# Kernel optimization log

Hardware: AMD Instinct MI355X
Metric: run time of the kernel (lower is better)

Reference implementation:

```python
import jax, jax.numpy as jnp
import numpy as np

IMG_H, IMG_W = 1024, 1024
STRIDES = (8, 16, 32, 64, 128)
NUM_CLASSES = 80
CONF_THR = 0.05
IOU_THR = 0.5
MAX_PER_CLASS = 100
MAX_DET = 100
K_CAND = 256  # candidates kept per class before greedy NMS (pre-sort cap)


def build_grids():
    gy, gx, gs = [], [], []
    for s in STRIDES:
        H, W = IMG_H // s, IMG_W // s
        h = jnp.arange(H, dtype=jnp.float32)
        w = jnp.arange(W, dtype=jnp.float32)
        gy_, gx_ = jnp.meshgrid(h, w)  # 'xy' indexing -> shape [W, H], matches tf.meshgrid
        gy.append(gy_.reshape(-1))
        gx.append(gx_.reshape(-1))
        gs.append(jnp.full((W * H,), float(s), dtype=jnp.float32))
    return jnp.concatenate(gy), jnp.concatenate(gx), jnp.concatenate(gs)


def pairwise_iou(b):
    # b: [K,4] as (y1, x1, y2, x2)
    y1, x1, y2, x2 = b[:, 0], b[:, 1], b[:, 2], b[:, 3]
    area = (y2 - y1) * (x2 - x1)
    ih = jnp.maximum(jnp.minimum(y2[:, None], y2[None, :]) - jnp.maximum(y1[:, None], y1[None, :]), 0.0)
    iw = jnp.maximum(jnp.minimum(x2[:, None], x2[None, :]) - jnp.maximum(x1[:, None], x1[None, :]), 0.0)
    inter = ih * iw
    union = area[:, None] + area[None, :] - inter
    return inter / jnp.maximum(union, 1e-8)


def nms_one_class(boxes, scores):
    # boxes [N,4], scores [N] -> (sel_boxes [MAX_PER_CLASS,4], sel_scores [MAX_PER_CLASS])
    top_s, idx = jax.lax.top_k(scores, K_CAND)
    cand = boxes[idx]                       # [K,4]
    valid = top_s > CONF_THR
    iou = jax.lax.stop_gradient(pairwise_iou(cand))  # suppression mask is non-differentiable
    rng = jnp.arange(K_CAND)

    def body(i, keep):
        sup = (iou[i] > IOU_THR) & (rng > i) & keep[i]
        return keep & ~sup

    keep = jax.lax.fori_loop(0, K_CAND, body, valid)
    kept = jnp.where(keep, top_s, 0.0)
    sel_s, sel_i = jax.lax.top_k(kept, MAX_PER_CLASS)
    return cand[sel_i], sel_s


def combined_nms(boxes, scores):
    # per image: boxes [N,4] shared across classes, scores [N,C]
    cls_boxes, cls_scores = jax.vmap(nms_one_class, in_axes=(None, 1))(boxes, scores)
    C = scores.shape[1]
    cls_labels = jnp.broadcast_to(jnp.arange(C, dtype=jnp.float32)[:, None], cls_scores.shape)
    flat_s = cls_scores.reshape(-1)
    flat_b = cls_boxes.reshape(-1, 4)
    flat_l = cls_labels.reshape(-1)
    fin_s, fin_i = jax.lax.top_k(flat_s, MAX_DET)
    fin_b = flat_b[fin_i] * (fin_s > 0.0)[:, None].astype(flat_b.dtype)  # zero pad boxes like TF
    fin_l = flat_l[fin_i]
    return fin_b, fin_l, fin_s


def decode(pred_regs, pred_ctrs, pred_clfs):
    gy, gx, gs = build_grids()
    gy, gx, gs = gy[:, None], gx[:, None], gs[:, None]     # [N,1]
    score = pred_clfs * pred_ctrs                           # [B,N,C]
    x1 = gx - pred_regs[..., 0:1]
    x2 = gx + pred_regs[..., 1:2]
    y1 = gy - pred_regs[..., 2:3]
    y2 = gy + pred_regs[..., 3:4]
    bbox = jnp.concatenate([y1, x1, y2, x2], axis=-1) * gs  # [B,N,4] in image coords
    return jax.vmap(combined_nms)(bbox, score)


def setup_inputs() -> dict:
    key = jax.random.key(0)
    k1, k2, k3 = jax.random.split(key, 3)
    N = sum((IMG_H // s) * (IMG_W // s) for s in STRIDES)  # 21824
    B = 16
    return {
        "pred_regs": jax.random.uniform(k1, (B, N, 4), jnp.float32),
        "pred_ctrs": jax.random.uniform(k2, (B, N, 1), jnp.float32),
        "pred_clfs": jax.random.uniform(k3, (B, N, NUM_CLASSES), jnp.float32),
    }


def reference(pred_regs, pred_ctrs, pred_clfs):
    # returns (final_bboxes [B,100,4], final_labels [B,100] float, final_scores [B,100])
    return decode(pred_regs, pred_ctrs, pred_clfs)
```

## Files before the change

kernel.cpp:

```cpp
#include <hip/hip_runtime.h>
#include <stdint.h>

#pragma clang fp contract(off)

namespace {
constexpr int kN = 21824;
constexpr int kB = 16;
constexpr int kC = 80;
constexpr int kK = 256;
constexpr int kMaxPC = 100;
constexpr int kMaxDet = 100;
constexpr int kBins1 = 2048;
constexpr int kCap = 1536;
constexpr int kSortN = 512;
constexpr int kRows = kB * kC;
constexpr int kTiles = kN / 64;
constexpr int kTPB = 6;
constexpr int kGScan = (kTiles + kTPB - 1) / kTPB;
constexpr int kLCap = 48;
constexpr float kThr = 0.72f;
}

__device__ __forceinline__ uint64_t make_key(float s, int n) {
  return ((uint64_t)__float_as_uint(s) << 16) | (uint32_t)(0xFFFF - n);
}

__device__ uint32_t block_scan_incl(uint32_t val) {
  __shared__ uint32_t wsum[4];
  int lane = threadIdx.x & 63;
  int wave = threadIdx.x >> 6;
  for (int d = 1; d < 64; d <<= 1) {
    uint32_t t = __shfl_up(val, (unsigned)d, 64);
    if (lane >= d) val += t;
  }
  if (lane == 63) wsum[wave] = val;
  __syncthreads();
  uint32_t off = 0;
  for (int w = 0; w < wave; ++w) off += wsum[w];
  __syncthreads();
  return val + off;
}

struct RegSrc {
  uint64_t k[6];
  int cnt;
  template <class F> __device__ void each(F f) const {
    #pragma unroll
    for (int j = 0; j < 6; ++j)
      if (j < cnt) f(k[j]);
  }
  template <class F> __device__ void each2(F f) const {
    #pragma unroll
    for (int j = 0; j < 6; ++j) f(k[j], j < cnt);
  }
};
struct ColSrc {
  const float* cl;
  const float* ct;
  template <class F> __device__ void each(F f) const {
    for (int n = threadIdx.x; n < kN; n += 256)
      f(make_key(cl[(size_t)n * kC] * ct[n], n));
  }
  template <class F> __device__ void each2(F f) const {
    constexpr int kNr = (kN + 255) & ~255;
    for (int n = threadIdx.x; n < kNr; n += 256) {
      bool v = n < kN;
      float s = v ? cl[(size_t)n * kC] * ct[n] : 0.0f;
      f(make_key(s, n), v);
    }
  }
};
struct ArrSrc {
  const float* s;
  int count;
  template <class F> __device__ void each(F f) const {
    for (int i = threadIdx.x; i < count; i += 256) f(make_key(s[i], i));
  }
  template <class F> __device__ void each2(F f) const {
    int cr = (count + 255) & ~255;
    for (int i = threadIdx.x; i < cr; i += 256) {
      bool v = i < count;
      float sv = v ? s[i] : 0.0f;
      f(make_key(sv, i), v);
    }
  }
};

template <class Src, bool FAST>
__device__ int refine_gather(const Src& src, int K, int cap,
                             uint32_t* hist, uint64_t* cbuf) {
  __shared__ int sel_bin;
  __shared__ uint32_t sel_hd, sel_above, qcnt;
  int tid = threadIdx.x;

  for (int i = tid; i < kBins1; i += 256) hist[i] = 0;
  __syncthreads();
  src.each([&](uint64_t k) {
    uint32_t bin = FAST ? (uint32_t)((k >> 28) & 0x7FF) : (uint32_t)(k >> 37);
    atomicAdd(&hist[bin], 1u);
  });
  __syncthreads();
  uint32_t krem = (uint32_t)K;
  {
    uint32_t bl[8], v = 0;
    int base = kBins1 - 1 - 8 * tid;
    for (int j = 0; j < 8; ++j) { bl[j] = hist[base - j]; v += bl[j]; }
    uint32_t S = block_scan_incl(v);
    if (S >= krem && (S - v) < krem) {
      uint32_t cum = S - v;
      for (int j = 0; j < 8; ++j) {
        cum += bl[j];
        if (cum >= krem) { sel_bin = base - j; sel_hd = bl[j]; sel_above = cum - bl[j]; break; }
      }
    }
    __syncthreads();
  }
  uint64_t prefix = FAST ? (uint64_t)(0x3F000u | (uint32_t)sel_bin)
                         : (uint64_t)sel_bin;
  int shift = FAST ? 28 : 37;
  krem = (uint32_t)K - sel_above;
  uint32_t Sge = ((uint32_t)K - krem) + sel_hd;
  __syncthreads();

  while (Sge > (uint32_t)cap) {
    int w = (shift > 8) ? 8 : shift;
    int ns = shift - w, bins = 1 << w, hs = shift;
    for (int i = tid; i < bins; i += 256) hist[i] = 0;
    __syncthreads();
    uint64_t pfx = prefix;
    src.each([&](uint64_t k) {
      if ((k >> hs) == pfx)
        atomicAdd(&hist[(uint32_t)(k >> ns) & (bins - 1)], 1u);
    });
    __syncthreads();
    uint32_t v = (tid < bins) ? hist[bins - 1 - tid] : 0;
    uint32_t S = block_scan_incl(v);
    if (v && S >= krem && (S - v) < krem) {
      sel_bin = bins - 1 - tid; sel_hd = v; sel_above = S - v;
    }
    __syncthreads();
    prefix = (prefix << w) | (uint32_t)sel_bin;
    krem -= sel_above;
    Sge = ((uint32_t)K - krem) + sel_hd;
    shift = ns;
    __syncthreads();
  }

  uint64_t L = prefix << shift;
  if (tid == 0) qcnt = 0;
  __syncthreads();
  {
    int lane = tid & 63;
    uint64_t lmask = (1ull << lane) - 1ull;
    src.each2([&](uint64_t k, bool valid) {
      bool q = valid && (k >= L);
      unsigned long long m = __ballot(q);
      uint32_t base = 0;
      if (lane == 0 && m) base = atomicAdd(&qcnt, (uint32_t)__popcll(m));
      base = __shfl(base, 0, 64);
      if (q) {
        uint32_t p = base + (uint32_t)__popcll(m & lmask);
        if (p < (uint32_t)cap) cbuf[p] = k;
      }
    });
  }
  __syncthreads();
  int Scnt = (int)qcnt;
  return Scnt > cap ? cap : Scnt;
}

__device__ __forceinline__ void bitonic512_desc(uint64_t* sortb) {
  int tid = threadIdx.x;
  uint64_t e0 = sortb[2 * tid], e1 = sortb[2 * tid + 1];
  #pragma unroll
  for (int k2 = 2; k2 <= kSortN; k2 <<= 1) {
    #pragma unroll
    for (int j = k2 >> 1; j >= 2; j >>= 1) {
      bool up = ((tid & (k2 >> 1)) == 0);
      uint64_t p0, p1;
      bool low;
      if (j >= 128) {
        __syncthreads();
        sortb[2 * tid] = e0; sortb[2 * tid + 1] = e1;
        __syncthreads();
        int pi = (2 * tid) ^ j;
        p0 = sortb[pi]; p1 = sortb[pi + 1];
        low = ((tid & (j >> 1)) == 0);
      } else {
        int d = j >> 1;
        p0 = (uint64_t)__shfl_xor((unsigned long long)e0, d, 64);
        p1 = (uint64_t)__shfl_xor((unsigned long long)e1, d, 64);
        low = ((tid & d) == 0);
      }
      bool keepMax = (up == low);
      e0 = (keepMax == (e0 > p0)) ? e0 : p0;
      e1 = (keepMax == (e1 > p1)) ? e1 : p1;
    }
    {
      bool up = ((tid & (k2 >> 1)) == 0);
      bool sw = up ? (e0 < e1) : (e0 > e1);
      uint64_t t0 = sw ? e1 : e0, t1 = sw ? e0 : e1;
      e0 = t0; e1 = t1;
    }
  }
  __syncthreads();
  sortb[2 * tid] = e0; sortb[2 * tid + 1] = e1;
  __syncthreads();
}

__global__ __launch_bounds__(256) void score_scan_kernel(
    const float* __restrict__ clfs, const float* __restrict__ ctrs,
    uint32_t* __restrict__ gcnt, uint64_t* __restrict__ glist) {
  int b = blockIdx.y;
  int t0 = blockIdx.x * kTPB;
  int t1 = t0 + kTPB; if (t1 > kTiles) t1 = kTiles;
  int nbase = t0 * 64;
  int nanch = (t1 - t0) * 64;

  __shared__ uint64_t lbuf[kC][kLCap + 1];
  __shared__ uint32_t lcnt[kC];
  __shared__ uint32_t gbase[kC];
  __shared__ float ct[kTPB * 64];
  int tid = threadIdx.x;
  for (int i = tid; i < kC; i += 256) lcnt[i] = 0;
  for (int i = tid; i < nanch; i += 256) ct[i] = ctrs[(size_t)b * kN + nbase + i];
  __syncthreads();

  const float4* src = (const float4*)(clfs + ((size_t)b * kN + nbase) * kC);
  int n4 = nanch * (kC / 4);
  float4 v = (tid < n4) ? src[tid] : float4{0, 0, 0, 0};
  for (int e = tid; e < n4; e += 256) {
    int en = e + 256;
    float4 vn = (en < n4) ? src[en] : float4{0, 0, 0, 0};
    int a = e / 20;
    int c0 = (e % 20) * 4;
    float cv = ct[a];
    int n = nbase + a;
    float sv[4] = {v.x * cv, v.y * cv, v.z * cv, v.w * cv};
    #pragma unroll
    for (int j = 0; j < 4; ++j) {
      if (sv[j] > kThr) {
        int c = c0 + j;
        uint32_t p = atomicAdd(&lcnt[c], 1u);
        if (p < kLCap) lbuf[c][p] = make_key(sv[j], n);
      }
    }
    v = vn;
  }
  __syncthreads();

  if (tid < kC) {
    uint32_t m = lcnt[tid];
    int row = b * kC + tid;
    if (m > kLCap) {
      atomicAdd(&gcnt[row], (uint32_t)(kCap + 1));
      gbase[tid] = 0xFFFFFFFFu;
    } else {
      gbase[tid] = m ? atomicAdd(&gcnt[row], m) : 0u;
    }
  }
  __syncthreads();

  int lane = tid & 63, wave = tid >> 6;
  for (int c = wave * 20; c < wave * 20 + 20; ++c) {
    uint32_t m = lcnt[c];
    uint32_t base = gbase[c];
    if (base == 0xFFFFFFFFu || m == 0) continue;
    if (m > kLCap) m = kLCap;
    int row = b * kC + c;
    for (uint32_t i = lane; i < m; i += 64) {
      uint32_t p = base + i;
      if (p < kCap) glist[(size_t)row * kCap + p] = lbuf[c][i];
    }
  }
}

__global__ __launch_bounds__(256) void nms_class_kernel(
    const uint32_t* __restrict__ gcnt, const uint64_t* __restrict__ glist,
    const float* __restrict__ clfs, const float* __restrict__ ctrs,
    const float* __restrict__ regs,
    float* __restrict__ cls_boxes, float* __restrict__ cls_scores) {
  int row = blockIdx.x;
  int b = row / kC, c = row % kC;
  int tid = threadIdx.x;
  int lane = tid & 63, wave = tid >> 6;

  __shared__ union alignas(16) {
    uint32_t hist[kBins1];
    uint64_t sortb[kSortN];
    uint32_t supm[kK][8];
  } hu;
  __shared__ float4 boxf4[kK];
  __shared__ float barea[kK];
  __shared__ uint64_t kinit[4];
  __shared__ uint64_t kfin[4];

  uint32_t cnt = gcnt[row];
  int Scnt;
  if (cnt >= (uint32_t)kK && cnt <= (uint32_t)kCap) {
    RegSrc rs; rs.cnt = 0;
    const uint64_t* gl = glist + (size_t)row * kCap;
    #pragma unroll
    for (int j = 0; j < 6; ++j) {
      int i = tid + j * 256;
      if (i < (int)cnt) { rs.k[j] = gl[i]; rs.cnt = j + 1; }
    }
    Scnt = refine_gather<RegSrc, true>(rs, kK, kSortN, hu.hist, hu.sortb);
  } else {
    ColSrc cs{clfs + (size_t)b * kN * kC + c, ctrs + (size_t)b * kN};
    Scnt = refine_gather<ColSrc, false>(cs, kK, kSortN, hu.hist, hu.sortb);
  }

  for (int i = Scnt + tid; i < kSortN; i += 256) hu.sortb[i] = 0;
  __syncthreads();
  bitonic512_desc(hu.sortb);
  uint64_t myk = hu.sortb[tid];
  __syncthreads();

  int n = 0xFFFF - (int)(myk & 0xFFFF);
  float sc_v = __uint_as_float((uint32_t)(myk >> 16));
  int off, hl;
  float sf;
  if (n < 16384)      { off = 0;     hl = 7; sf = 8.f;   }
  else if (n < 20480) { off = 16384; hl = 6; sf = 16.f;  }
  else if (n < 21504) { off = 20480; hl = 5; sf = 32.f;  }
  else if (n < 21760) { off = 21504; hl = 4; sf = 64.f;  }
  else                { off = 21760; hl = 3; sf = 128.f; }
  int kk = n - off;
  float gx = (float)(kk >> hl);
  float gy = (float)(kk & ((1 << hl) - 1));
  const float4 r = ((const float4*)regs)[(size_t)b * kN + n];
  float4 mybox;
  mybox.x = (gy - r.z) * sf;
  mybox.y = (gx - r.x) * sf;
  mybox.z = (gy + r.w) * sf;
  mybox.w = (gx + r.y) * sf;
  float my_a = (mybox.z - mybox.x) * (mybox.w - mybox.y);
  boxf4[tid] = mybox;
  barea[tid] = my_a;
  unsigned long long vm = __ballot(sc_v > 0.05f);
  if (lane == 0) kinit[wave] = vm;
  {
    uint64_t* sp = (uint64_t*)&hu.supm[0][0];
    #pragma unroll
    for (int q = 0; q < 4; ++q) sp[tid + q * 256] = 0;
  }
  __syncthreads();

  {
    int tw = tid >> 5;
    uint32_t meq = 0xFFFFFFFEu << (tid & 31);
    for (int w = wave << 1; w < 8; ++w) {
      const float4* bp = boxf4 + (w << 5);
      const float* ap = barea + (w << 5);
      uint32_t cur = 0;
      #pragma unroll
      for (int s = 0; s < 32; ++s) {
        const float4 Bx = bp[s];
        float aB = ap[s];
        float yy1 = fmaxf(mybox.x, Bx.x);
        float yy2 = fminf(mybox.z, Bx.z);
        float xx1 = fmaxf(mybox.y, Bx.y);
        float xx2 = fminf(mybox.w, Bx.w);
        float ih = fmaxf(yy2 - yy1, 0.0f);
        float iw = fmaxf(xx2 - xx1, 0.0f);
        float inter = ih * iw;
        float un = (aB + my_a) - inter;
        float unc = fmaxf(un, 1e-8f);
        cur |= (inter + inter > unc) ? (1u << s) : 0u;
      }
      uint32_t mask = (w > tw) ? 0xFFFFFFFFu : ((w == tw) ? meq : 0u);
      if (mask) hu.supm[tid][w] = cur & mask;
    }
  }
  __syncthreads();

  if (wave == 0) {
    uint64_t kw0 = kinit[0], kw1 = kinit[1], kw2 = kinit[2], kw3 = kinit[3];
    #define NMS_SECTION(W, KW)                                              \
      _Pragma("unroll")                                                     \
      for (int ch = 0; ch < 16; ++ch) {                                     \
        const ulonglong2* s0 = (const ulonglong2*)hu.supm[(W << 6) + ch * 4 + 0]; \
        const ulonglong2* s1 = (const ulonglong2*)hu.supm[(W << 6) + ch * 4 + 1]; \
        const ulonglong2* s2 = (const ulonglong2*)hu.supm[(W << 6) + ch * 4 + 2]; \
        const ulonglong2* s3 = (const ulonglong2*)hu.supm[(W << 6) + ch * 4 + 3]; \
        ulonglong2 aL = s0[0], aH = s0[1];                                  \
        ulonglong2 bL = s1[0], bH = s1[1];                                  \
        ulonglong2 cL = s2[0], cH = s2[1];                                  \
        ulonglong2 dL = s3[0], dH = s3[1];                                  \
        if ((KW >> (ch * 4 + 0)) & 1ull) { kw0 &= ~aL.x; kw1 &= ~aL.y; kw2 &= ~aH.x; kw3 &= ~aH.y; } \
        if ((KW >> (ch * 4 + 1)) & 1ull) { kw0 &= ~bL.x; kw1 &= ~bL.y; kw2 &= ~bH.x; kw3 &= ~bH.y; } \
        if ((KW >> (ch * 4 + 2)) & 1ull) { kw0 &= ~cL.x; kw1 &= ~cL.y; kw2 &= ~cH.x; kw3 &= ~cH.y; } \
        if ((KW >> (ch * 4 + 3)) & 1ull) { kw0 &= ~dL.x; kw1 &= ~dL.y; kw2 &= ~dH.x; kw3 &= ~dH.y; } \
      }
    NMS_SECTION(0, kw0)
    NMS_SECTION(1, kw1)
    NMS_SECTION(2, kw2)
    NMS_SECTION(3, kw3)
    #undef NMS_SECTION
    if (lane == 0) { kfin[0] = kw0; kfin[1] = kw1; kfin[2] = kw2; kfin[3] = kw3; }
  }
  __syncthreads();

  uint64_t kw0 = kfin[0], kw1 = kfin[1], kw2 = kfin[2], kw3 = kfin[3];
  uint64_t ww = (wave == 0) ? kw0 : (wave == 1) ? kw1 : (wave == 2) ? kw2 : kw3;
  bool keptf = (ww >> lane) & 1ull;
  int kept_total = (int)(__popcll(kw0) + __popcll(kw1) +
                         __popcll(kw2) + __popcll(kw3));
  int kept_before = (int)__popcll(ww & ((1ull << lane) - 1ull));
  if (wave > 0) kept_before += (int)__popcll(kw0);
  if (wave > 1) kept_before += (int)__popcll(kw1);
  if (wave > 2) kept_before += (int)__popcll(kw2);

  int rank2 = keptf ? kept_before : (kept_total + tid - kept_before);
  if (rank2 < kMaxPC) {
    float ks = keptf ? sc_v : 0.0f;
    size_t obase = ((size_t)row) * kMaxPC + rank2;
    cls_scores[obase] = ks;
    float* ob = cls_boxes + obase * 4;
    ob[0] = mybox.x; ob[1] = mybox.y; ob[2] = mybox.z; ob[3] = mybox.w;
  }
}

__global__ __launch_bounds__(256) void final_topk_kernel(
    const float* __restrict__ cls_scores, const float* __restrict__ cls_boxes,
    float* __restrict__ out) {
  int b = blockIdx.x;
  int tid = threadIdx.x;
  const int M = kC * kMaxPC;
  __shared__ union alignas(16) {
    uint32_t hist[kBins1];
    uint64_t sortb[kSortN];
  } hu;

  ArrSrc as{cls_scores + (size_t)b * M, M};
  int Scnt = refine_gather<ArrSrc, false>(as, kMaxDet, kSortN, hu.hist, hu.sortb);

  for (int i = Scnt + tid; i < kSortN; i += 256) hu.sortb[i] = 0;
  __syncthreads();
  bitonic512_desc(hu.sortb);

  if (tid < kMaxDet) {
    uint64_t myk = hu.sortb[tid];
    float sv = __uint_as_float((uint32_t)(myk >> 16));
    int f = 0xFFFF - (int)(myk & 0xFFFF);
    int cls = f / 100;
    const float* bp = cls_boxes + ((size_t)b * M + f) * 4;
    float m = (sv > 0.0f) ? 1.0f : 0.0f;
    float* ob = out + ((size_t)b * kMaxDet + tid) * 4;
    ob[0] = bp[0] * m; ob[1] = bp[1] * m; ob[2] = bp[2] * m; ob[3] = bp[3] * m;
    out[(size_t)kB * kMaxDet * 4 + (size_t)b * kMaxDet + tid] = (float)cls;
    out[(size_t)kB * kMaxDet * 5 + (size_t)b * kMaxDet + tid] = sv;
  }
}

extern "C" void kernel_launch(void* const* d_in, const int* in_sizes, int n_in,
                              void* d_out, int out_size, void* d_ws, size_t ws_size,
                              hipStream_t stream) {
  (void)in_sizes; (void)n_in; (void)out_size;
  const float* regs = (const float*)d_in[0];
  const float* ctrs = (const float*)d_in[1];
  const float* clfs = (const float*)d_in[2];
  float* out = (float*)d_out;

  const size_t glB  = (size_t)kRows * kCap * sizeof(uint64_t);
  const size_t cbB  = (size_t)kRows * kMaxPC * 4 * sizeof(float);
  const size_t csB  = (size_t)kRows * kMaxPC * sizeof(float);
  const size_t cntB = 8192;
  if (ws_size < glB + cbB + csB + cntB) return;

  char* p = (char*)d_ws;
  uint64_t* glist   = (uint64_t*)p; p += glB;
  float* cls_boxes  = (float*)p;    p += cbB;
  float* cls_scores = (float*)p;    p += csB;
  uint32_t* gcnt    = (uint32_t*)p;

  hipMemsetAsync(gcnt, 0, (size_t)kRows * sizeof(uint32_t), stream);
  score_scan_kernel<<<dim3(kGScan, kB), 256, 0, stream>>>(clfs, ctrs, gcnt, glist);
  nms_class_kernel<<<kRows, 256, 0, stream>>>(gcnt, glist, clfs, ctrs, regs,
                                              cls_boxes, cls_scores);
  final_topk_kernel<<<kB, 256, 0, stream>>>(cls_scores, cls_boxes, out);
}
```

Measured before the change: 270.5 us.

## Balance IoU mask tasks across threads and skip all-zero suppression rows

The upper-triangular IoU bitmask work is flattened into 1152 (row, word) tasks spread evenly across the 256 threads, replacing the per-thread loop whose length depended on the wave. Each row that has any suppression bit sets a flag in a shared bitmap through an atomic OR. The serial wave-0 NMS sweep then skips groups of four rows that are all zero, avoiding their LDS loads. In exchange it adds shared atomics, a little index arithmetic per task, and a branch in the unrolled sweep.

```diff
diff --git a/kernel.cpp b/kernel.cpp
--- a/kernel.cpp
+++ b/kernel.cpp
@@ -19,6 +19,7 @@
 constexpr int kGScan = (kTiles + kTPB - 1) / kTPB;
 constexpr int kLCap = 48;
 constexpr float kThr = 0.72f;
+constexpr int kTasks = 1152;
 }
 
 __device__ __forceinline__ uint64_t make_key(float s, int n) {
@@ -292,6 +293,7 @@
   } hu;
   __shared__ float4 boxf4[kK];
   __shared__ float barea[kK];
+  __shared__ uint32_t rnz[8];
   __shared__ uint64_t kinit[4];
   __shared__ uint64_t kfin[4];
 
@@ -344,59 +346,69 @@
     uint64_t* sp = (uint64_t*)&hu.supm[0][0];
     #pragma unroll
     for (int q = 0; q < 4; ++q) sp[tid + q * 256] = 0;
-  }
-  __syncthreads();
-
-  {
-    int tw = tid >> 5;
-    uint32_t meq = 0xFFFFFFFEu << (tid & 31);
-    for (int w = wave << 1; w < 8; ++w) {
-      const float4* bp = boxf4 + (w << 5);
-      const float* ap = barea + (w << 5);
-      uint32_t cur = 0;
-      #pragma unroll
-      for (int s = 0; s < 32; ++s) {
-        const float4 Bx = bp[s];
-        float aB = ap[s];
-        float yy1 = fmaxf(mybox.x, Bx.x);
-        float yy2 = fminf(mybox.z, Bx.z);
-        float xx1 = fmaxf(mybox.y, Bx.y);
-        float xx2 = fminf(mybox.w, Bx.w);
-        float ih = fmaxf(yy2 - yy1, 0.0f);
-        float iw = fmaxf(xx2 - xx1, 0.0f);
-        float inter = ih * iw;
-        float un = (aB + my_a) - inter;
-        float unc = fmaxf(un, 1e-8f);
-        cur |= (inter + inter > unc) ? (1u << s) : 0u;
-      }
-      uint32_t mask = (w > tw) ? 0xFFFFFFFFu : ((w == tw) ? meq : 0u);
-      if (mask) hu.supm[tid][w] = cur & mask;
-    }
+    if (tid < 8) rnz[tid] = 0;
+  }
+  __syncthreads();
+
+  for (int t = tid; t < kTasks; t += 256) {
+    int w = (t >= 32) + (t >= 96) + (t >= 192) + (t >= 320) +
+            (t >= 480) + (t >= 672) + (t >= 896);
+    int rr = t - 16 * w * (w + 1);
+    float4 A = boxf4[rr];
+    float aA = barea[rr];
+    const float4* bp = boxf4 + (w << 5);
+    const float* ap = barea + (w << 5);
+    uint32_t cur = 0;
+    #pragma unroll
+    for (int s = 0; s < 32; ++s) {
+      const float4 Bx = bp[s];
+      float aB = ap[s];
+      float yy1 = fmaxf(A.x, Bx.x);
+      float yy2 = fminf(A.z, Bx.z);
+      float xx1 = fmaxf(A.y, Bx.y);
+      float xx2 = fminf(A.w, Bx.w);
+      float ih = fmaxf(yy2 - yy1, 0.0f);
+      float iw = fmaxf(xx2 - xx1, 0.0f);
+      float inter = ih * iw;
+      float un = (aB + aA) - inter;
+      float unc = fmaxf(un, 1e-8f);
+      cur |= (inter + inter > unc) ? (1u << s) : 0u;
+    }
+    uint32_t mask = (w == (rr >> 5)) ? (0xFFFFFFFEu << (rr & 31)) : 0xFFFFFFFFu;
+    cur &= mask;
+    hu.supm[rr][w] = cur;
+    if (cur) atomicOr(&rnz[rr >> 5], 1u << (rr & 31));
   }
   __syncthreads();
 
   if (wave == 0) {
     uint64_t kw0 = kinit[0], kw1 = kinit[1], kw2 = kinit[2], kw3 = kinit[3];
-    #define NMS_SECTION(W, KW)                                              \
+    uint64_t wn0 = rnz[0] | ((uint64_t)rnz[1] << 32);
+    uint64_t wn1 = rnz[2] | ((uint64_t)rnz[3] << 32);
+    uint64_t wn2 = rnz[4] | ((uint64_t)rnz[5] << 32);
+    uint64_t wn3 = rnz[6] | ((uint64_t)rnz[7] << 32);
+    #define NMS_SECTION(W, KW, WN)                                          \
       _Pragma("unroll")                                                     \
       for (int ch = 0; ch < 16; ++ch) {                                     \
-        const ulonglong2* s0 = (const ulonglong2*)hu.supm[(W << 6) + ch * 4 + 0]; \
-        const ulonglong2* s1 = (const ulonglong2*)hu.supm[(W << 6) + ch * 4 + 1]; \
-        const ulonglong2* s2 = (const ulonglong2*)hu.supm[(W << 6) + ch * 4 + 2]; \
-        const ulonglong2* s3 = (const ulonglong2*)hu.supm[(W << 6) + ch * 4 + 3]; \
-        ulonglong2 aL = s0[0], aH = s0[1];                                  \
-        ulonglong2 bL = s1[0], bH = s1[1];                                  \
-        ulonglong2 cL = s2[0], cH = s2[1];                                  \
-        ulonglong2 dL = s3[0], dH = s3[1];                                  \
-        if ((KW >> (ch * 4 + 0)) & 1ull) { kw0 &= ~aL.x; kw1 &= ~aL.y; kw2 &= ~aH.x; kw3 &= ~aH.y; } \
-        if ((KW >> (ch * 4 + 1)) & 1ull) { kw0 &= ~bL.x; kw1 &= ~bL.y; kw2 &= ~bH.x; kw3 &= ~bH.y; } \
-        if ((KW >> (ch * 4 + 2)) & 1ull) { kw0 &= ~cL.x; kw1 &= ~cL.y; kw2 &= ~cH.x; kw3 &= ~cH.y; } \
-        if ((KW >> (ch * 4 + 3)) & 1ull) { kw0 &= ~dL.x; kw1 &= ~dL.y; kw2 &= ~dH.x; kw3 &= ~dH.y; } \
+        if ((WN >> (ch * 4)) & 0xFull) {                                    \
+          const ulonglong2* s0 = (const ulonglong2*)hu.supm[(W << 6) + ch * 4 + 0]; \
+          const ulonglong2* s1 = (const ulonglong2*)hu.supm[(W << 6) + ch * 4 + 1]; \
+          const ulonglong2* s2 = (const ulonglong2*)hu.supm[(W << 6) + ch * 4 + 2]; \
+          const ulonglong2* s3 = (const ulonglong2*)hu.supm[(W << 6) + ch * 4 + 3]; \
+          ulonglong2 aL = s0[0], aH = s0[1];                                \
+          ulonglong2 bL = s1[0], bH = s1[1];                                \
+          ulonglong2 cL = s2[0], cH = s2[1];                                \
+          ulonglong2 dL = s3[0], dH = s3[1];                                \
+          if ((KW >> (ch * 4 + 0)) & 1ull) { kw0 &= ~aL.x; kw1 &= ~aL.y; kw2 &= ~aH.x; kw3 &= ~aH.y; } \
+          if ((KW >> (ch * 4 + 1)) & 1ull) { kw0 &= ~bL.x; kw1 &= ~bL.y; kw2 &= ~bH.x; kw3 &= ~bH.y; } \
+          if ((KW >> (ch * 4 + 2)) & 1ull) { kw0 &= ~cL.x; kw1 &= ~cL.y; kw2 &= ~cH.x; kw3 &= ~cH.y; } \
+          if ((KW >> (ch * 4 + 3)) & 1ull) { kw0 &= ~dL.x; kw1 &= ~dL.y; kw2 &= ~dH.x; kw3 &= ~dH.y; } \
+        }                                                                   \
       }
-    NMS_SECTION(0, kw0)
-    NMS_SECTION(1, kw1)
-    NMS_SECTION(2, kw2)
-    NMS_SECTION(3, kw3)
+    NMS_SECTION(0, kw0, wn0)
+    NMS_SECTION(1, kw1, wn1)
+    NMS_SECTION(2, kw2, wn2)
+    NMS_SECTION(3, kw3, wn3)
     #undef NMS_SECTION
     if (lane == 0) { kfin[0] = kw0; kfin[1] = kw1; kfin[2] = kw2; kfin[3] = kw3; }
   }
```

After: 242.9 us. -10.2%, faster.
